# Kernel tuning notes

Measured on AMD Instinct MI355X. Metric: run time of the kernel, lower is better.

The kernel has to match this reference:

```python
import jax, jax.numpy as jnp
import numpy as np

N_PARTICLES = 6000
BOX_LENGTH = 10.0  # nm, orthogonal box
CUTOFF = 0.5       # nm


def _pair_indices(n):
    # static upper-triangular (i < j) pair list, matching meshgrid + (i < j) mask
    i_idx, j_idx = np.triu_indices(n, k=1)
    return jnp.asarray(i_idx.astype(np.int32)), jnp.asarray(j_idx.astype(np.int32))


def setup_inputs() -> dict:
    key = jax.random.key(0)
    k_pos, = jax.random.split(key, 1)
    positions = jax.random.uniform(k_pos, (N_PARTICLES, 3), dtype=jnp.float32) * BOX_LENGTH
    # orthogonal box: only the diagonal is read by the displacement function
    box_vectors = jnp.diag(jnp.array([BOX_LENGTH, BOX_LENGTH, BOX_LENGTH], dtype=jnp.float32))
    return {"positions": positions, "box_vectors": box_vectors, "is_periodic": 1}


def reference(positions, box_vectors, is_periodic):
    """Brute N^2 neighborlist (only_unique_pairs=True path).

    Faithful math: r_ij = pos[i]-pos[j]; PBC minimum-image wrap via remainder;
    d_ij = ||r_ij||; cutoff mask. The torch original boolean-compacts to a
    data-dependent n_pairs; for jit-compatible static shapes we keep the full
    P = n(n-1)/2 pair axis and mask: out-of-cutoff pair indices are -1 and
    their d_ij / r_ij are zeroed. In-cutoff entries are bitwise identical to
    the compacted torch outputs.
    """
    n = positions.shape[0]
    i_idx, j_idx = _pair_indices(n)

    r_ij = positions[i_idx] - positions[j_idx]          # [P, 3]
    if is_periodic:
        box_lengths = jnp.diag(box_vectors)             # [3]
        half = box_lengths * 0.5
        r_ij = jnp.remainder(r_ij + half, box_lengths) - half
    d_ij = jnp.sqrt(jnp.sum(r_ij * r_ij, axis=1, keepdims=True))  # [P, 1]

    in_cutoff = d_ij <= CUTOFF                          # [P, 1]
    pair_indices = jnp.where(in_cutoff[:, 0],
                             jnp.stack([i_idx, j_idx]).astype(jnp.int64),
                             -1)                        # [2, P]
    d_out = jnp.where(in_cutoff, d_ij, 0.0)
    r_out = jnp.where(in_cutoff, r_ij, 0.0)
    return pair_indices, d_out, r_out
```

## Files before the change

### kernel.cpp

```cpp
#include <hip/hip_runtime.h>


constexpr int NPART  = 6000;
constexpr int NPAIRS = 17997000;
constexpr float CUT  = 0.5f;

__device__ __forceinline__ int row_start(int i) {
    return i * (NPART - 1) - (i * (i - 1)) / 2;
}

__device__ __forceinline__ float pbc_wrap(float r, float b, float h) {
    float v = __fadd_rn(r, h);
    if (v >= b)      v = __fsub_rn(v, b);
    else if (v < 0.f) v = __fadd_rn(v, b);
    return __fsub_rn(v, h);
}

__global__ __launch_bounds__(256) void nbl_kernel(
    const float* __restrict__ pos,
    const float* __restrict__ boxv,
    const int*  __restrict__ is_per,
    float* __restrict__ out)
{
    int p = (blockIdx.x * blockDim.x + threadIdx.x) * 4;
    if (p >= NPAIRS) return;

    const float A = 2.0f * NPART - 1.0f;
    float disc = A * A - 8.0f * (float)p;
    int i = (int)((A - sqrtf(disc)) * 0.5f);
    if (i < 0) i = 0;
    if (i > NPART - 2) i = NPART - 2;
    while (i < NPART - 2 && row_start(i + 1) <= p) ++i;
    while (i > 0 && row_start(i) > p) --i;
    int j = i + 1 + (p - row_start(i));

    const bool per = (*is_per != 0);
    const float bx = boxv[0], by = boxv[4], bz = boxv[8];
    const float hx = __fmul_rn(bx, 0.5f);
    const float hy = __fmul_rn(by, 0.5f);
    const float hz = __fmul_rn(bz, 0.5f);

    float xi = pos[3 * i + 0], yi = pos[3 * i + 1], zi = pos[3 * i + 2];

    float oi[4], oj[4], od[4], orr[12];

    #pragma unroll
    for (int k = 0; k < 4; ++k) {
        float xj = pos[3 * j + 0], yj = pos[3 * j + 1], zj = pos[3 * j + 2];
        float rx = __fsub_rn(xi, xj);
        float ry = __fsub_rn(yi, yj);
        float rz = __fsub_rn(zi, zj);
        if (per) {
            rx = pbc_wrap(rx, bx, hx);
            ry = pbc_wrap(ry, by, hy);
            rz = pbc_wrap(rz, bz, hz);
        }
        float s = __fadd_rn(__fadd_rn(__fmul_rn(rx, rx), __fmul_rn(ry, ry)),
                            __fmul_rn(rz, rz));
        float d = __fsqrt_rn(s);
        bool in = (d <= CUT);

        oi[k] = in ? (float)i : -1.0f;
        oj[k] = in ? (float)j : -1.0f;
        od[k] = in ? d : 0.0f;
        orr[3 * k + 0] = in ? rx : 0.0f;
        orr[3 * k + 1] = in ? ry : 0.0f;
        orr[3 * k + 2] = in ? rz : 0.0f;

        ++j;
        if (j == NPART) { ++i; j = i + 1;
            xi = pos[3 * i + 0]; yi = pos[3 * i + 1]; zi = pos[3 * i + 2]; }
    }

    *(float4*)(out + p)              = make_float4(oi[0], oi[1], oi[2], oi[3]);
    *(float4*)(out + NPAIRS + p)     = make_float4(oj[0], oj[1], oj[2], oj[3]);
    *(float4*)(out + 2 * NPAIRS + p) = make_float4(od[0], od[1], od[2], od[3]);
    float* rb = out + 3 * NPAIRS + 3 * p;
    *(float4*)(rb + 0) = make_float4(orr[0], orr[1], orr[2],  orr[3]);
    *(float4*)(rb + 4) = make_float4(orr[4], orr[5], orr[6],  orr[7]);
    *(float4*)(rb + 8) = make_float4(orr[8], orr[9], orr[10], orr[11]);
}

extern "C" void kernel_launch(void* const* d_in, const int* in_sizes, int n_in,
                              void* d_out, int out_size, void* d_ws, size_t ws_size,
                              hipStream_t stream) {
    const float* pos    = (const float*)d_in[0];
    const float* boxv   = (const float*)d_in[1];
    const int*   is_per = (const int*)d_in[2];
    float* out = (float*)d_out;

    const int block = 256;
    const int nthreads = NPAIRS / 4;
    const int grid = (nthreads + block - 1) / block;
    nbl_kernel<<<grid, block, 0, stream>>>(pos, boxv, is_per, out);
}
```

Measured before the change: 434.7 us.

## Prefill outputs with memsets and scatter only in-cutoff pairs from a per-pair kernel

Fills the index region with -1.0f and the distance/vector region with zeros using async memsets, then launches one thread per pair that writes only the pairs within the cutoff. Most pairs fall outside the cutoff, so the compute kernel's stores become sparse. In exchange, the work drops from four pairs per thread to one, which loses the vectorized float4 stores and multiplies the row-search sqrt work by four. The memsets still write the full output, and the remaining scattered stores are uncoalesced.

Measured after the change: 469.4 us. 8.0% more time.

```diff
diff --git a/kernel.cpp b/kernel.cpp
--- a/kernel.cpp
+++ b/kernel.cpp
@@ -4,6 +4,7 @@
 constexpr int NPART  = 6000;
 constexpr int NPAIRS = 17997000;
 constexpr float CUT  = 0.5f;
+constexpr int TPB = 256;
 
 __device__ __forceinline__ int row_start(int i) {
     return i * (NPART - 1) - (i * (i - 1)) / 2;
@@ -11,74 +12,51 @@
 
 __device__ __forceinline__ float pbc_wrap(float r, float b, float h) {
     float v = __fadd_rn(r, h);
-    if (v >= b)      v = __fsub_rn(v, b);
+    if (v >= b)       v = __fsub_rn(v, b);
     else if (v < 0.f) v = __fadd_rn(v, b);
     return __fsub_rn(v, h);
 }
 
-__global__ __launch_bounds__(256) void nbl_kernel(
+__global__ __launch_bounds__(TPB) void nbl_scatter_kernel(
     const float* __restrict__ pos,
     const float* __restrict__ boxv,
     const int*  __restrict__ is_per,
     float* __restrict__ out)
 {
-    int p = (blockIdx.x * blockDim.x + threadIdx.x) * 4;
+    const int p = blockIdx.x * TPB + threadIdx.x;
     if (p >= NPAIRS) return;
 
-    const float A = 2.0f * NPART - 1.0f;
-    float disc = A * A - 8.0f * (float)p;
-    int i = (int)((A - sqrtf(disc)) * 0.5f);
+    int disc_i = 143976001 - 8 * p;
+    float sq = sqrtf((float)disc_i);
+    int i = (int)((11999.0f - sq) * 0.5f);
     if (i < 0) i = 0;
     if (i > NPART - 2) i = NPART - 2;
     while (i < NPART - 2 && row_start(i + 1) <= p) ++i;
     while (i > 0 && row_start(i) > p) --i;
-    int j = i + 1 + (p - row_start(i));
+    const int j = i + 1 + (p - row_start(i));
 
-    const bool per = (*is_per != 0);
-    const float bx = boxv[0], by = boxv[4], bz = boxv[8];
-    const float hx = __fmul_rn(bx, 0.5f);
-    const float hy = __fmul_rn(by, 0.5f);
-    const float hz = __fmul_rn(bz, 0.5f);
+    float rx = __fsub_rn(pos[3 * i + 0], pos[3 * j + 0]);
+    float ry = __fsub_rn(pos[3 * i + 1], pos[3 * j + 1]);
+    float rz = __fsub_rn(pos[3 * i + 2], pos[3 * j + 2]);
 
-    float xi = pos[3 * i + 0], yi = pos[3 * i + 1], zi = pos[3 * i + 2];
-
-    float oi[4], oj[4], od[4], orr[12];
-
-    #pragma unroll
-    for (int k = 0; k < 4; ++k) {
-        float xj = pos[3 * j + 0], yj = pos[3 * j + 1], zj = pos[3 * j + 2];
-        float rx = __fsub_rn(xi, xj);
-        float ry = __fsub_rn(yi, yj);
-        float rz = __fsub_rn(zi, zj);
-        if (per) {
-            rx = pbc_wrap(rx, bx, hx);
-            ry = pbc_wrap(ry, by, hy);
-            rz = pbc_wrap(rz, bz, hz);
-        }
-        float s = __fadd_rn(__fadd_rn(__fmul_rn(rx, rx), __fmul_rn(ry, ry)),
-                            __fmul_rn(rz, rz));
-        float d = __fsqrt_rn(s);
-        bool in = (d <= CUT);
-
-        oi[k] = in ? (float)i : -1.0f;
-        oj[k] = in ? (float)j : -1.0f;
-        od[k] = in ? d : 0.0f;
-        orr[3 * k + 0] = in ? rx : 0.0f;
-        orr[3 * k + 1] = in ? ry : 0.0f;
-        orr[3 * k + 2] = in ? rz : 0.0f;
-
-        ++j;
-        if (j == NPART) { ++i; j = i + 1;
-            xi = pos[3 * i + 0]; yi = pos[3 * i + 1]; zi = pos[3 * i + 2]; }
+    if (*is_per != 0) {
+        const float bx = boxv[0], by = boxv[4], bz = boxv[8];
+        rx = pbc_wrap(rx, bx, __fmul_rn(bx, 0.5f));
+        ry = pbc_wrap(ry, by, __fmul_rn(by, 0.5f));
+        rz = pbc_wrap(rz, bz, __fmul_rn(bz, 0.5f));
     }
 
-    *(float4*)(out + p)              = make_float4(oi[0], oi[1], oi[2], oi[3]);
-    *(float4*)(out + NPAIRS + p)     = make_float4(oj[0], oj[1], oj[2], oj[3]);
-    *(float4*)(out + 2 * NPAIRS + p) = make_float4(od[0], od[1], od[2], od[3]);
-    float* rb = out + 3 * NPAIRS + 3 * p;
-    *(float4*)(rb + 0) = make_float4(orr[0], orr[1], orr[2],  orr[3]);
-    *(float4*)(rb + 4) = make_float4(orr[4], orr[5], orr[6],  orr[7]);
-    *(float4*)(rb + 8) = make_float4(orr[8], orr[9], orr[10], orr[11]);
+    float s = __fadd_rn(__fadd_rn(__fmul_rn(rx, rx), __fmul_rn(ry, ry)),
+                        __fmul_rn(rz, rz));
+    float d = __fsqrt_rn(s);
+
+    if (d <= CUT) {
+        out[p]              = (float)i;
+        out[NPAIRS + p]     = (float)j;
+        out[2 * NPAIRS + p] = d;
+        float* rb = out + 3 * NPAIRS + 3 * p;
+        rb[0] = rx; rb[1] = ry; rb[2] = rz;
+    }
 }
 
 extern "C" void kernel_launch(void* const* d_in, const int* in_sizes, int n_in,
@@ -89,8 +67,11 @@
     const int*   is_per = (const int*)d_in[2];
     float* out = (float*)d_out;
 
-    const int block = 256;
-    const int nthreads = NPAIRS / 4;
-    const int grid = (nthreads + block - 1) / block;
-    nbl_kernel<<<grid, block, 0, stream>>>(pos, boxv, is_per, out);
+    hipMemsetD32Async((hipDeviceptr_t)out, (int)0xBF800000,
+                      (size_t)2 * NPAIRS, stream);
+    hipMemsetAsync(out + (size_t)2 * NPAIRS, 0,
+                   (size_t)4 * NPAIRS * sizeof(float), stream);
+
+    const int grid = (NPAIRS + TPB - 1) / TPB;
+    nbl_scatter_kernel<<<grid, TPB, 0, stream>>>(pos, boxv, is_per, out);
 }
```
